# Optimization experiments

Measured on AMD Instinct MI355X. Metric: run time of the kernel, lower is better.

The kernel has to match this reference:

```python
import jax, jax.numpy as jnp
import numpy as np

H = 768


def lstm_cell(x, h, c, Wih, Whh, b):
    # PyTorch LSTMCell gate order: i, f, g, o
    gates = x @ Wih.T + h @ Whh.T + b
    i, f, g, o = jnp.split(gates, 4, axis=-1)
    c = jax.nn.sigmoid(f) * c + jax.nn.sigmoid(i) * jnp.tanh(g)
    h = jax.nn.sigmoid(o) * jnp.tanh(c)
    return h, c


def run_lstm(x, Wih, Whh, b, reverse):
    B = x.shape[0]
    Hd = Whh.shape[1]
    def step(carry, xt):
        h, c = lstm_cell(xt, carry[0], carry[1], Wih, Whh, b)
        return (h, c), h
    init = (jnp.zeros((B, Hd), x.dtype), jnp.zeros((B, Hd), x.dtype))
    _, hs = jax.lax.scan(step, init, jnp.swapaxes(x, 0, 1), reverse=reverse)
    return jnp.swapaxes(hs, 0, 1)


def _forward(hidden_state, golds, lstm_Wih_f, lstm_Whh_f, lstm_b_f,
             lstm_Wih_b, lstm_Whh_b, lstm_b_b, subw_Wih, subw_Whh, subw_b,
             word_Wih, word_Whh, word_b, cls_W, cls_b):
    B, T, _ = hidden_state.shape
    dt = hidden_state.dtype
    out_f = run_lstm(hidden_state, lstm_Wih_f, lstm_Whh_f, lstm_b_f, False)
    out_b = run_lstm(hidden_state, lstm_Wih_b, lstm_Whh_b, lstm_b_b, True)
    lstm_out = jnp.concatenate([out_f, out_b], -1)  # [B, T, 2H]

    subw_map = jnp.array([1, 2, 2], dtype=jnp.int32)
    word_map = jnp.array([0, 1, 1], dtype=jnp.int32)
    bidx = jnp.arange(B)
    S1, S2 = 2 * T + 2, T + 1
    carry0 = (jnp.zeros((S1, B, H), dt), jnp.zeros((S1, B, H), dt), jnp.zeros((B,), jnp.int32),
              jnp.zeros((S2, B, H), dt), jnp.zeros((S2, B, H), dt), jnp.zeros((B,), jnp.int32))
    xs = (jnp.swapaxes(lstm_out[:, :T - 1], 0, 1),  # features for subword cell at step idx-1
          jnp.swapaxes(lstm_out[:, 1:T], 0, 1),     # features concatenated into cls at step idx
          golds[:, 1:T].T.astype(jnp.int32))

    def step(carry, x):
        sh, sc, spos, wh, wc, wpos = carry
        x_prev, x_cur, g = x
        # subword stack-LSTM: read top-of-stack state, push new state at pos+1
        h1, c1 = lstm_cell(x_prev, sh[spos, bidx], sc[spos, bidx], subw_Wih, subw_Whh, subw_b)
        sh = sh.at[spos + 1, bidx].set(h1)
        sc = sc.at[spos + 1, bidx].set(c1)
        subword = jnp.concatenate([h1, c1], -1)  # [B, 2H] input to word stack-LSTM
        # word stack-LSTM
        h2, c2 = lstm_cell(subword, wh[wpos, bidx], wc[wpos, bidx], word_Wih, word_Whh, word_b)
        wh = wh.at[wpos + 1, bidx].set(h2)
        wc = wc.at[wpos + 1, bidx].set(c2)
        out = jnp.concatenate([h2, x_cur], -1) @ cls_W.T + cls_b  # [B, 2]
        # training path: ops from gold actions
        sop = subw_map[g]
        wop = word_map[g]
        spos = jnp.where(sop == 1, spos + 1, 0)      # APP: push; SEP: clear subword stack
        wpos = jnp.where(wop == 1, wpos + 1, wpos)   # SEP: push word; APP: hold
        return (sh, sc, spos, wh, wc, wpos), out

    _, outs = jax.lax.scan(step, carry0, xs)  # [T-1, B, 2]
    pred0 = jnp.broadcast_to(jnp.asarray([-1.0, 1.0], dt), (1, B, 2))
    return jnp.swapaxes(jnp.concatenate([pred0, outs], 0), 0, 1)  # [B, T, 2]


def setup_inputs() -> dict:
    key = jax.random.key(0)
    ks = jax.random.split(key, 12)
    B, T = 64, 256
    s = 0.02
    W = lambda k, shape: jax.random.normal(k, shape, jnp.float32) * s
    return {
        "hidden_state": jax.random.normal(ks[0], (B, T, H), jnp.float32),
        "golds": jax.random.randint(ks[1], (B, T), 0, 2),
        "lstm_Wih_f": W(ks[2], (4 * H, H)), "lstm_Whh_f": W(ks[3], (4 * H, H)), "lstm_b_f": jnp.zeros((4 * H,), jnp.float32),
        "lstm_Wih_b": W(ks[4], (4 * H, H)), "lstm_Whh_b": W(ks[5], (4 * H, H)), "lstm_b_b": jnp.zeros((4 * H,), jnp.float32),
        "subw_Wih": W(ks[6], (4 * H, 2 * H)), "subw_Whh": W(ks[7], (4 * H, H)), "subw_b": jnp.zeros((4 * H,), jnp.float32),
        "word_Wih": W(ks[8], (4 * H, 2 * H)), "word_Whh": W(ks[9], (4 * H, H)), "word_b": jnp.zeros((4 * H,), jnp.float32),
        "cls_W": W(ks[10], (2, 3 * H)), "cls_b": jnp.zeros((2,), jnp.float32),
    }


def reference(hidden_state, golds, lstm_Wih_f, lstm_Whh_f, lstm_b_f,
              lstm_Wih_b, lstm_Whh_b, lstm_b_b, subw_Wih, subw_Whh, subw_b,
              word_Wih, word_Whh, word_b, cls_W, cls_b):
    return _forward(hidden_state, golds, lstm_Wih_f, lstm_Whh_f, lstm_b_f,
                    lstm_Wih_b, lstm_Whh_b, lstm_b_b, subw_Wih, subw_Whh, subw_b,
                    word_Wih, word_Whh, word_b, cls_W, cls_b)
```

## Files before the change

### kernel.cpp

```cpp
#include <hip/hip_runtime.h>
#include <hip/hip_bf16.h>

typedef __attribute__((ext_vector_type(8))) short bf16x8;
typedef __attribute__((ext_vector_type(4))) float f32x4;
typedef __attribute__((ext_vector_type(4))) unsigned u32x4;

#define HD   768
#define NB   64
#define NT   256
#define NGATE 3072
#define FPAD 32

__device__ __forceinline__ float fast_sig(float x) { return 1.f / (1.f + __expf(-x)); }
__device__ __forceinline__ float fast_tanh(float x) {
  float t = __expf(-2.f * fabsf(x));
  float r = (1.f - t) / (1.f + t);
  return x < 0.f ? -r : r;
}
__device__ __forceinline__ float bf2f(unsigned short u) {
  union { unsigned i; float f; } v; v.i = ((unsigned)u) << 16; return v.f;
}
__device__ __forceinline__ unsigned short f2bfu(float f) {
  union { __hip_bfloat16 b; unsigned short u; } c;
  c.b = __float2bfloat16(f);
  return c.u;
}
__device__ __forceinline__ unsigned pack2(float a, float b) {
  return (unsigned)f2bfu(a) | ((unsigned)f2bfu(b) << 16);
}

#define VMW(N) do { asm volatile("s_waitcnt vmcnt(" #N ")" ::: "memory"); \
                    __builtin_amdgcn_sched_barrier(0); } while (0)

__device__ __forceinline__ int aload(int* p) {
  return __hip_atomic_load(p, __ATOMIC_RELAXED, __HIP_MEMORY_SCOPE_AGENT);
}
__device__ __forceinline__ void ustore(unsigned* p, unsigned v) {
  __hip_atomic_store(p, v, __ATOMIC_RELAXED, __HIP_MEMORY_SCOPE_AGENT);
}
__device__ __forceinline__ u32x4 cload16(const char* p) {
  u32x4 r;
  asm volatile("global_load_dwordx4 %0, %1, off sc0 sc1"
               : "=v"(r) : "v"(p) : "memory");
  return r;
}

__device__ __forceinline__ void arrive_flag(int* f) {
  asm volatile("s_waitcnt vmcnt(0)" ::: "memory");
  __syncthreads();
  if (threadIdx.x == 0)
    __hip_atomic_fetch_add(f, 1, __ATOMIC_RELAXED, __HIP_MEMORY_SCOPE_AGENT);
}

__device__ __forceinline__ void wait2(int* fa, int ta, int* fb, int tb) {
  int tid = threadIdx.x;
  int* p = nullptr; int tgt = 0;
  if (tid < 96)                            { p = fa + tid * FPAD;         tgt = ta; }
  else if (fb && tid >= 128 && tid < 224)  { p = fb + (tid - 128) * FPAD; tgt = tb; }
  if (p && tgt > 0) {
    int guard = 0;
    while (aload(p) < tgt) {
      __builtin_amdgcn_s_sleep(1);
      if (++guard > (1 << 17)) break;
    }
  }
  __syncthreads();
}

__device__ __forceinline__ int frag_dw(int b, int j) {
  return (((((j >> 5) * 4 + (b >> 4)) * 4 + ((j >> 3) & 3)) * 16 + (b & 15)) * 4)
         + ((j & 7) >> 1);
}

__device__ __forceinline__ int wswz(int r) {
  return ((r & 7) << 4) | (((r >> 3) & 3) << 7);
}

__device__ __forceinline__ void load_W_lds(unsigned short* Wl,
                                           const __hip_bfloat16* Wg,
                                           int n_base, int K)
{
  int chunksPerRow = (K * 2) / 16;
  int total = 32 * chunksPerRow;
  for (int idx = threadIdx.x; idx < total; idx += 256) {
    int r  = idx / chunksPerRow;
    int cb = (idx % chunksPerRow) * 16;
    bf16x8 v = *(const bf16x8*)((const char*)(Wg + (long)(n_base + r) * K) + cb);
    *(bf16x8*)((char*)Wl + (long)r * (K * 2) + (cb ^ wswz(r))) = v;
  }
}

__device__ __forceinline__ void mfma_cached(
    const __hip_bfloat16* a0p, int kbase, int NIT,
    const char* w0, const char* w1, int xr0, int xr1, int kk,
    f32x4& acc0, f32x4& acc1)
{
  #pragma unroll 4
  for (int it = kbase; it < kbase + NIT; ++it) {
    bf16x8 av = *(const bf16x8*)(a0p + it * 32 + kk);
    int oo = (it * 32 + kk) * 2;
    bf16x8 bv0 = *(const bf16x8*)(w0 + (oo ^ xr0));
    bf16x8 bv1 = *(const bf16x8*)(w1 + (oo ^ xr1));
    acc0 = __builtin_amdgcn_mfma_f32_16x16x32_bf16(av, bv0, acc0, 0, 0, 0);
    acc1 = __builtin_amdgcn_mfma_f32_16x16x32_bf16(av, bv1, acc1, 0, 0, 0);
  }
}

__device__ __forceinline__ void issue12(u32x4* dst, const char* base, int c0) {
  #pragma unroll
  for (int i = 0; i < 12; ++i)
    dst[i] = cload16(base + (size_t)(c0 + i) * 4096);
}

__device__ __forceinline__ void mfma_st12(
    const u32x4* st, int kbase,
    const char* w0, const char* w1, int xr0, int xr1, int kk,
    f32x4& acc0, f32x4& acc1)
{
  #pragma unroll
  for (int i = 0; i < 12; ++i) {
    int oo = ((kbase + i) * 32 + kk) * 2;
    bf16x8 av = __builtin_bit_cast(bf16x8, st[i]);
    bf16x8 bv0 = *(const bf16x8*)(w0 + (oo ^ xr0));
    bf16x8 bv1 = *(const bf16x8*)(w1 + (oo ^ xr1));
    acc0 = __builtin_amdgcn_mfma_f32_16x16x32_bf16(av, bv0, acc0, 0, 0, 0);
    acc1 = __builtin_amdgcn_mfma_f32_16x16x32_bf16(av, bv1, acc1, 0, 0, 0);
  }
}

__device__ __forceinline__ void pack_seg(const float* Wih, const float* Whh,
                                         __hip_bfloat16* dst, int Kih,
                                         long id0, long stride)
{
  int K = Kih + HD;
  long total = (long)NGATE * K;
  for (long idx = id0; idx < total; idx += stride) {
    int np = (int)(idx / K), k = (int)(idx % K);
    int j = np >> 2, g = np & 3;
    int n = g * HD + j;
    float v = (k < Kih) ? Wih[(long)n * Kih + k] : Whh[(long)n * HD + (k - Kih)];
    dst[idx] = __float2bfloat16(v);
  }
}

__global__ void setup_kernel(
    const float* __restrict__ x,
    const float* __restrict__ WihF, const float* __restrict__ WhhF,
    const float* __restrict__ WihB, const float* __restrict__ WhhB,
    const float* __restrict__ WihS, const float* __restrict__ WhhS,
    const float* __restrict__ WihW, const float* __restrict__ WhhW,
    __hip_bfloat16* __restrict__ X16,
    __hip_bfloat16* __restrict__ WF, __hip_bfloat16* __restrict__ WB,
    __hip_bfloat16* __restrict__ WS, __hip_bfloat16* __restrict__ WW)
{
  long id0 = (long)blockIdx.x * blockDim.x + threadIdx.x;
  long stride = (long)gridDim.x * blockDim.x;
  for (long i = id0; i < (long)NB * NT * HD; i += stride)
    X16[i] = __float2bfloat16(x[i]);
  pack_seg(WihF, WhhF, WF, 768, id0, stride);
  pack_seg(WihB, WhhB, WB, 768, id0, stride);
  pack_seg(WihS, WhhS, WS, 1536, id0, stride);
  pack_seg(WihW, WhhW, WW, 1536, id0, stride);
}

__global__ void fill_sentinel(float* out, int n, float v)
{
  int i = blockIdx.x * blockDim.x + threadIdx.x;
  if (i < n) out[i] = v;
}

__global__ __launch_bounds__(256, 1) void bilstm_persist(
    const __hip_bfloat16* __restrict__ X16,
    const __hip_bfloat16* __restrict__ WF,
    const __hip_bfloat16* __restrict__ WB,
    const float* __restrict__ bF, const float* __restrict__ bB,
    unsigned* __restrict__ H16u,
    __hip_bfloat16* __restrict__ L16,
    int* __restrict__ flags)
{
  __shared__ unsigned short Wl[32 * 1536];
  __shared__ float gl[64][33];
  int blk = blockIdx.x, dir = blk / 96, nt = blk % 96;
  load_W_lds(Wl, dir ? WB : WF, nt * 32, 1536);
  const float* bias = dir ? bB : bF;
  int* myflags = flags + dir * 96 * FPAD;
  int tid = threadIdx.x;
  unsigned* L16u = (unsigned*)L16;

  int w = tid >> 6, l = tid & 63, lr = l & 15, lh = l >> 4;
  const char* w0 = (const char*)Wl + lr * 3072;
  const char* w1 = (const char*)Wl + (16 + lr) * 3072;
  int xr0 = wswz(lr), xr1 = wswz(16 + lr);
  int kk = 8 * lh;
  int bA = 16 * w + lr;

  int e0 = tid * 2;
  int b = e0 >> 3, jj = e0 & 7;
  int j0 = nt * 8 + jj;
  float bv[2][4];
  #pragma unroll
  for (int u = 0; u < 2; ++u) {
    bv[u][0] = bias[j0 + u];          bv[u][1] = bias[HD + j0 + u];
    bv[u][2] = bias[2 * HD + j0 + u]; bv[u][3] = bias[3 * HD + j0 + u];
  }
  int fdw = frag_dw(b, j0);
  float cst[2] = {0.f, 0.f};
  __syncthreads();

  for (int s = 0; s < NT; ++s) {
    int par = s & 1;
    int t = dir ? (NT - 1 - s) : s;
    const __hip_bfloat16* xb = X16 + (long)t * HD + (long)bA * (NT * HD);
    f32x4 acc0 = {0.f, 0.f, 0.f, 0.f};
    f32x4 acc1 = {0.f, 0.f, 0.f, 0.f};
    mfma_cached(xb, 0, 12, w0, w1, xr0, xr1, kk, acc0, acc1);
    if (s > 0) wait2(myflags, s, nullptr, 0);
    const char* fpH = (const char*)(H16u + (long)(par * 2 + dir) * 24576)
                      + (size_t)(w * 64 + l) * 16;
    u32x4 hA[12], hB[12];
    issue12(hA, fpH, 0);
    issue12(hB, fpH, 12);
    mfma_cached(xb, 12, 12, w0, w1, xr0, xr1, kk, acc0, acc1);
    VMW(0);
    mfma_st12(hA, 24, w0, w1, xr0, xr1, kk, acc0, acc1);
    mfma_st12(hB, 36, w0, w1, xr0, xr1, kk, acc0, acc1);
    #pragma unroll
    for (int r = 0; r < 4; ++r) {
      gl[16 * w + 4 * lh + r][lr]      = acc0[r];
      gl[16 * w + 4 * lh + r][16 + lr] = acc1[r];
    }
    __syncthreads();
    float hv[2];
    #pragma unroll
    for (int u = 0; u < 2; ++u) {
      int col = 4 * (jj + u);
      float vi = gl[b][col + 0] + bv[u][0];
      float vf = gl[b][col + 1] + bv[u][1];
      float vg = gl[b][col + 2] + bv[u][2];
      float vo = gl[b][col + 3] + bv[u][3];
      float si = fast_sig(vi), sf = fast_sig(vf), so = fast_sig(vo);
      float tg = fast_tanh(vg);
      float c = sf * cst[u] + si * tg;
      cst[u] = c;
      hv[u] = so * fast_tanh(c);
    }
    unsigned pk = pack2(hv[0], hv[1]);
    ustore(H16u + (long)((par ^ 1) * 2 + dir) * 24576 + fdw, pk);
    L16u[((long)b * NT + t) * 768 + dir * 384 + (j0 >> 1)] = pk;
    if (s < NT - 1) arrive_flag(myflags + nt * FPAD);
  }
}

__global__ __launch_bounds__(256) void clsx_kernel(
    const __hip_bfloat16* __restrict__ L16,
    const float* __restrict__ clsW, const float* __restrict__ clsb,
    float* __restrict__ out)
{
  int t = blockIdx.x;
  int tid = threadIdx.x;
  int b = tid >> 2, o = (tid >> 1) & 1, hh = tid & 1;
  if (t == 0) {
    if (hh == 0) out[((long)b * NT) * 2 + o] = o ? 1.f : -1.f;
    return;
  }
  const bf16x8* xp = (const bf16x8*)(L16 + ((long)b * NT + t) * 1536 + hh * 768);
  const float* wv = clsW + o * 2304 + HD + hh * 768;
  float s = 0.f;
  for (int k = 0; k < 96; ++k) {
    bf16x8 v = xp[k];
    #pragma unroll
    for (int e = 0; e < 8; ++e)
      s += bf2f((unsigned short)v[e]) * wv[k * 8 + e];
  }
  s += __shfl_down(s, 1);
  if (hh == 0) out[((long)b * NT + t) * 2 + o] = s + clsb[o];
}

__global__ __launch_bounds__(256, 1) void stack_persist(
    const __hip_bfloat16* __restrict__ L16,
    const __hip_bfloat16* __restrict__ WS,
    const __hip_bfloat16* __restrict__ WW,
    const float* __restrict__ bS, const float* __restrict__ bW,
    const int* __restrict__ golds,
    const float* __restrict__ clsW,
    unsigned* __restrict__ H1Su,
    unsigned* __restrict__ H2Su,
    unsigned* __restrict__ SUBWu,
    float* __restrict__ out,
    int* __restrict__ flags)
{
  __shared__ unsigned short Wl[32 * 2304];
  __shared__ float gl[64][33];
  int blk = blockIdx.x, role = blk / 96, nt = blk % 96;
  int* flagS = flags + 2 * 96 * FPAD;
  int* flagW = flags + 3 * 96 * FPAD;
  const float* bias = role ? bW : bS;
  load_W_lds(Wl, role ? WW : WS, nt * 32, 2304);
  int tid = threadIdx.x;

  int w = tid >> 6, l = tid & 63, lr = l & 15, lh = l >> 4;
  const char* w0 = (const char*)Wl + lr * 4608;
  const char* w1 = (const char*)Wl + (16 + lr) * 4608;
  int xr0 = wswz(lr), xr1 = wswz(16 + lr);
  int kk = 8 * lh;
  int bA = 16 * w + lr;

  int e0 = tid * 2;
  int b = e0 >> 3, jj = e0 & 7;
  int j0 = nt * 8 + jj;
  float bv[2][4];
  #pragma unroll
  for (int u = 0; u < 2; ++u) {
    bv[u][0] = bias[j0 + u];          bv[u][1] = bias[HD + j0 + u];
    bv[u][2] = bias[2 * HD + j0 + u]; bv[u][3] = bias[3 * HD + j0 + u];
  }
  const int* gp = golds + b * NT + 1;
  int fdw_h = frag_dw(b, j0);
  float cst[2] = {0.f, 0.f};
  float hreg[2] = {0.f, 0.f};
  __syncthreads();

  if (role == 0) {
    int fdw_c = frag_dw(b, 768 + j0);
    for (int s = 0; s < NT - 1; ++s) {
      int g = gp[s];
      const __hip_bfloat16* lb = L16 + (long)s * 1536 + (long)bA * (NT * 1536);
      f32x4 acc0 = {0.f, 0.f, 0.f, 0.f};
      f32x4 acc1 = {0.f, 0.f, 0.f, 0.f};
      mfma_cached(lb, 0, 24, w0, w1, xr0, xr1, kk, acc0, acc1);
      wait2(flagS, s, flagW, s - 3);
      const char* fpH1 = (const char*)(H1Su + (long)(s & 1) * 24576)
                         + (size_t)(w * 64 + l) * 16;
      u32x4 hA[12], hB[12];
      issue12(hA, fpH1, 0);
      issue12(hB, fpH1, 12);
      mfma_cached(lb, 24, 24, w0, w1, xr0, xr1, kk, acc0, acc1);
      VMW(0);
      mfma_st12(hA, 48, w0, w1, xr0, xr1, kk, acc0, acc1);
      mfma_st12(hB, 60, w0, w1, xr0, xr1, kk, acc0, acc1);
      #pragma unroll
      for (int r = 0; r < 4; ++r) {
        gl[16 * w + 4 * lh + r][lr]      = acc0[r];
        gl[16 * w + 4 * lh + r][16 + lr] = acc1[r];
      }
      __syncthreads();
      float h1v[2], c1v[2];
      #pragma unroll
      for (int u = 0; u < 2; ++u) {
        int col = 4 * (jj + u);
        float vi = gl[b][col + 0] + bv[u][0];
        float vf = gl[b][col + 1] + bv[u][1];
        float vg = gl[b][col + 2] + bv[u][2];
        float vo = gl[b][col + 3] + bv[u][3];
        float si = fast_sig(vi), sf = fast_sig(vf), so = fast_sig(vo);
        float tg = fast_tanh(vg);
        c1v[u] = sf * cst[u] + si * tg;
        h1v[u] = so * fast_tanh(c1v[u]);
      }
      bool push = (g == 0);
      unsigned pkh = pack2(h1v[0], h1v[1]);
      unsigned pkc = pack2(c1v[0], c1v[1]);
      unsigned* sb = SUBWu + (long)(s & 3) * 49152;
      ustore(sb + fdw_h, pkh);
      ustore(sb + fdw_c, pkc);
      ustore(H1Su + (long)((s + 1) & 1) * 24576 + fdw_h, push ? pkh : 0u);
      cst[0] = push ? c1v[0] : 0.f;
      cst[1] = push ? c1v[1] : 0.f;
      arrive_flag(flagS + nt * FPAD);
    }
  } else {
    float cw0[2], cw1[2];
    #pragma unroll
    for (int u = 0; u < 2; ++u) { cw0[u] = clsW[j0 + u]; cw1[u] = clsW[2304 + j0 + u]; }
    for (int s = 0; s < NT - 1; ++s) {
      int g = gp[s];
      wait2(flagW, s, nullptr, 0);
      const char* fpH = (const char*)(H2Su + (long)(s & 1) * 24576)
                        + (size_t)(w * 64 + l) * 16;
      const char* fpS = (const char*)(SUBWu + (long)(s & 3) * 49152)
                        + (size_t)(w * 64 + l) * 16;
      u32x4 sA[12], sB[12], sC[12];
      issue12(sA, fpH, 0);
      issue12(sB, fpH, 12);
      wait2(flagS, s + 1, nullptr, 0);
      issue12(sC, fpS, 0);
      f32x4 acc0 = {0.f, 0.f, 0.f, 0.f};
      f32x4 acc1 = {0.f, 0.f, 0.f, 0.f};
      VMW(24);
      mfma_st12(sA, 48, w0, w1, xr0, xr1, kk, acc0, acc1);
      issue12(sA, fpS, 12);
      VMW(24);
      mfma_st12(sB, 60, w0, w1, xr0, xr1, kk, acc0, acc1);
      issue12(sB, fpS, 24);
      VMW(24);
      mfma_st12(sC, 0, w0, w1, xr0, xr1, kk, acc0, acc1);
      issue12(sC, fpS, 36);
      VMW(24);
      mfma_st12(sA, 12, w0, w1, xr0, xr1, kk, acc0, acc1);
      VMW(12);
      mfma_st12(sB, 24, w0, w1, xr0, xr1, kk, acc0, acc1);
      VMW(0);
      mfma_st12(sC, 36, w0, w1, xr0, xr1, kk, acc0, acc1);
      #pragma unroll
      for (int r = 0; r < 4; ++r) {
        gl[16 * w + 4 * lh + r][lr]      = acc0[r];
        gl[16 * w + 4 * lh + r][16 + lr] = acc1[r];
      }
      __syncthreads();
      float p0 = 0.f, p1 = 0.f;
      float h2v[2], c2v[2];
      #pragma unroll
      for (int u = 0; u < 2; ++u) {
        int col = 4 * (jj + u);
        float vi = gl[b][col + 0] + bv[u][0];
        float vf = gl[b][col + 1] + bv[u][1];
        float vg = gl[b][col + 2] + bv[u][2];
        float vo = gl[b][col + 3] + bv[u][3];
        float si = fast_sig(vi), sf = fast_sig(vf), so = fast_sig(vo);
        float tg = fast_tanh(vg);
        c2v[u] = sf * cst[u] + si * tg;
        h2v[u] = so * fast_tanh(c2v[u]);
        p0 += h2v[u] * cw0[u];
        p1 += h2v[u] * cw1[u];
      }
      bool push = (g >= 1);
      #pragma unroll
      for (int u = 0; u < 2; ++u) {
        cst[u]  = push ? c2v[u] : cst[u];
        hreg[u] = push ? h2v[u] : hreg[u];
      }
      ustore(H2Su + (long)((s + 1) & 1) * 24576 + fdw_h, pack2(hreg[0], hreg[1]));
      p0 += __shfl_down(p0, 1); p1 += __shfl_down(p1, 1);
      p0 += __shfl_down(p0, 2); p1 += __shfl_down(p1, 2);
      if ((tid & 3) == 0) {
        int bb = tid >> 2;
        atomicAdd(&out[((long)bb * NT + s + 1) * 2 + 0], p0);
        atomicAdd(&out[((long)bb * NT + s + 1) * 2 + 1], p1);
      }
      if (s < NT - 2) arrive_flag(flagW + nt * FPAD);
    }
  }
}

extern "C" void kernel_launch(void* const* d_in, const int* in_sizes, int n_in,
                              void* d_out, int out_size, void* d_ws, size_t ws_size,
                              hipStream_t stream)
{
  const float* x     = (const float*)d_in[0];
  const int*   golds = (const int*)d_in[1];
  const float* WihF  = (const float*)d_in[2];
  const float* WhhF  = (const float*)d_in[3];
  const float* bF    = (const float*)d_in[4];
  const float* WihB  = (const float*)d_in[5];
  const float* WhhB  = (const float*)d_in[6];
  const float* bB    = (const float*)d_in[7];
  const float* WihS  = (const float*)d_in[8];
  const float* WhhS  = (const float*)d_in[9];
  const float* bS    = (const float*)d_in[10];
  const float* WihW  = (const float*)d_in[11];
  const float* WhhW  = (const float*)d_in[12];
  const float* bW    = (const float*)d_in[13];
  const float* clsW  = (const float*)d_in[14];
  const float* clsb  = (const float*)d_in[15];
  float* out = (float*)d_out;

  const size_t OFF_X16  = 0;
  const size_t OFF_WF   = 25165824;
  const size_t OFF_WB   = 34603008;
  const size_t OFF_WS   = 44040192;
  const size_t OFF_WW   = 58195968;
  const size_t OFF_L16  = 72351744;
  const size_t OFF_H16  = 122683392;
  const size_t OFF_H1S  = 123076608;
  const size_t OFF_H2S  = 123273216;
  const size_t OFF_SUBW = 123469824;
  const size_t OFF_FLG  = 124256256;
  const size_t WS_NEEDED = 124305408;

  if (ws_size < WS_NEEDED) {
    fill_sentinel<<<(out_size + 255) / 256, 256, 0, stream>>>(out, out_size, 12345.f);
    return;
  }

  char* ws = (char*)d_ws;
  __hip_bfloat16* X16  = (__hip_bfloat16*)(ws + OFF_X16);
  __hip_bfloat16* WF   = (__hip_bfloat16*)(ws + OFF_WF);
  __hip_bfloat16* WB   = (__hip_bfloat16*)(ws + OFF_WB);
  __hip_bfloat16* WSp  = (__hip_bfloat16*)(ws + OFF_WS);
  __hip_bfloat16* WWp  = (__hip_bfloat16*)(ws + OFF_WW);
  __hip_bfloat16* L16  = (__hip_bfloat16*)(ws + OFF_L16);
  unsigned*       H16u = (unsigned*)(ws + OFF_H16);
  unsigned*       H1Su = (unsigned*)(ws + OFF_H1S);
  unsigned*       H2Su = (unsigned*)(ws + OFF_H2S);
  unsigned*       SUBWu= (unsigned*)(ws + OFF_SUBW);
  int*            flags= (int*)(ws + OFF_FLG);

  setup_kernel<<<4096, 256, 0, stream>>>(x, WihF, WhhF, WihB, WhhB,
                                         WihS, WhhS, WihW, WhhW,
                                         X16, WF, WB, WSp, WWp);
  hipMemsetAsync(ws + OFF_H16, 0, WS_NEEDED - OFF_H16, stream);

  bilstm_persist<<<192, 256, 0, stream>>>(X16, WF, WB, bF, bB, H16u, L16, flags);

  clsx_kernel<<<NT, 256, 0, stream>>>(L16, clsW, clsb, out);

  stack_persist<<<192, 256, 0, stream>>>(L16, WSp, WWp, bS, bW, golds, clsW,
                                         H1Su, H2Su, SUBWu, out, flags);
}
```

Before: 4.145 ms.

## Fuse classifier into stack kernel with extra reducer blocks, replace atomics with partial buffer

Removes the separate clsx_kernel launch and folds its work into 64 extra blocks of stack_persist. Those blocks compute the lstm_out classifier term and then reduce per-step partial logits from a new OUTC buffer, replacing the atomicAdd accumulation. The buffer reuses the X16 workspace region. The recurrent h-fragment loads are also restructured into a double-buffered mfma_frag helper. The aim is to cut a launch and atomic contention, but the reducer blocks poll flags and add occupancy pressure alongside the persistent blocks.

Result: faster. 3.884 ms (-6.3%).

```diff
diff --git a/kernel.cpp b/kernel.cpp
--- a/kernel.cpp
+++ b/kernel.cpp
@@ -38,9 +38,18 @@
 __device__ __forceinline__ void ustore(unsigned* p, unsigned v) {
   __hip_atomic_store(p, v, __ATOMIC_RELAXED, __HIP_MEMORY_SCOPE_AGENT);
 }
+__device__ __forceinline__ void ustore64(unsigned long long* p, unsigned long long v) {
+  __hip_atomic_store(p, v, __ATOMIC_RELAXED, __HIP_MEMORY_SCOPE_AGENT);
+}
 __device__ __forceinline__ u32x4 cload16(const char* p) {
   u32x4 r;
   asm volatile("global_load_dwordx4 %0, %1, off sc0 sc1"
+               : "=v"(r) : "v"(p) : "memory");
+  return r;
+}
+__device__ __forceinline__ unsigned cload4(const char* p) {
+  unsigned r;
+  asm volatile("global_load_dword %0, %1, off sc0 sc1"
                : "=v"(r) : "v"(p) : "memory");
   return r;
 }
@@ -67,6 +76,18 @@
   __syncthreads();
 }
 
+__device__ __forceinline__ void wait_coarse(int* fa, int t) {
+  int tid = threadIdx.x;
+  if (tid < 96) {
+    int guard = 0;
+    while (aload(fa + tid * FPAD) < t) {
+      __builtin_amdgcn_s_sleep(127);
+      if (++guard > (1 << 15)) break;
+    }
+  }
+  __syncthreads();
+}
+
 __device__ __forceinline__ int frag_dw(int b, int j) {
   return (((((j >> 5) * 4 + (b >> 4)) * 4 + ((j >> 3) & 3)) * 16 + (b & 15)) * 4)
          + ((j & 7) >> 1);
@@ -103,6 +124,40 @@
     bf16x8 bv1 = *(const bf16x8*)(w1 + (oo ^ xr1));
     acc0 = __builtin_amdgcn_mfma_f32_16x16x32_bf16(av, bv0, acc0, 0, 0, 0);
     acc1 = __builtin_amdgcn_mfma_f32_16x16x32_bf16(av, bv1, acc1, 0, 0, 0);
+  }
+}
+
+template<int CF>
+__device__ __forceinline__ void mfma_frag(
+    const char* Fbase, int l, int w,
+    const char* w0, const char* w1, int xr0, int xr1, int kk, int kbase,
+    f32x4& acc0, f32x4& acc1)
+{
+  const char* fp = Fbase + (size_t)(w * 64 + l) * 16;
+  u32x4 st[2][12];
+  #pragma unroll
+  for (int i = 0; i < 12; ++i)
+    st[0][i] = cload16(fp + (size_t)i * 4096);
+  #pragma unroll
+  for (int c = 0; c < CF / 12; ++c) {
+    if (c + 1 < CF / 12) {
+      #pragma unroll
+      for (int i = 0; i < 12; ++i)
+        st[(c + 1) & 1][i] = cload16(fp + (size_t)((c + 1) * 12 + i) * 4096);
+      asm volatile("s_waitcnt vmcnt(12)" ::: "memory");
+    } else {
+      asm volatile("s_waitcnt vmcnt(0)" ::: "memory");
+    }
+    __builtin_amdgcn_sched_barrier(0);
+    #pragma unroll
+    for (int i = 0; i < 12; ++i) {
+      int oo = ((kbase + c * 12 + i) * 32 + kk) * 2;
+      bf16x8 av = __builtin_bit_cast(bf16x8, st[c & 1][i]);
+      bf16x8 bv0 = *(const bf16x8*)(w0 + (oo ^ xr0));
+      bf16x8 bv1 = *(const bf16x8*)(w1 + (oo ^ xr1));
+      acc0 = __builtin_amdgcn_mfma_f32_16x16x32_bf16(av, bv0, acc0, 0, 0, 0);
+      acc1 = __builtin_amdgcn_mfma_f32_16x16x32_bf16(av, bv1, acc1, 0, 0, 0);
+    }
   }
 }
 
@@ -210,20 +265,13 @@
   for (int s = 0; s < NT; ++s) {
     int par = s & 1;
     int t = dir ? (NT - 1 - s) : s;
-    const __hip_bfloat16* xb = X16 + (long)t * HD + (long)bA * (NT * HD);
     f32x4 acc0 = {0.f, 0.f, 0.f, 0.f};
     f32x4 acc1 = {0.f, 0.f, 0.f, 0.f};
-    mfma_cached(xb, 0, 12, w0, w1, xr0, xr1, kk, acc0, acc1);
+    mfma_cached(X16 + (long)t * HD + (long)bA * (NT * HD), 0, 24,
+                w0, w1, xr0, xr1, kk, acc0, acc1);
     if (s > 0) wait2(myflags, s, nullptr, 0);
-    const char* fpH = (const char*)(H16u + (long)(par * 2 + dir) * 24576)
-                      + (size_t)(w * 64 + l) * 16;
-    u32x4 hA[12], hB[12];
-    issue12(hA, fpH, 0);
-    issue12(hB, fpH, 12);
-    mfma_cached(xb, 12, 12, w0, w1, xr0, xr1, kk, acc0, acc1);
-    VMW(0);
-    mfma_st12(hA, 24, w0, w1, xr0, xr1, kk, acc0, acc1);
-    mfma_st12(hB, 36, w0, w1, xr0, xr1, kk, acc0, acc1);
+    mfma_frag<24>((const char*)(H16u + (long)(par * 2 + dir) * 24576),
+                  l, w, w0, w1, xr0, xr1, kk, 24, acc0, acc1);
     #pragma unroll
     for (int r = 0; r < 4; ++r) {
       gl[16 * w + 4 * lh + r][lr]      = acc0[r];
@@ -251,41 +299,17 @@
   }
 }
 
-__global__ __launch_bounds__(256) void clsx_kernel(
-    const __hip_bfloat16* __restrict__ L16,
-    const float* __restrict__ clsW, const float* __restrict__ clsb,
-    float* __restrict__ out)
-{
-  int t = blockIdx.x;
-  int tid = threadIdx.x;
-  int b = tid >> 2, o = (tid >> 1) & 1, hh = tid & 1;
-  if (t == 0) {
-    if (hh == 0) out[((long)b * NT) * 2 + o] = o ? 1.f : -1.f;
-    return;
-  }
-  const bf16x8* xp = (const bf16x8*)(L16 + ((long)b * NT + t) * 1536 + hh * 768);
-  const float* wv = clsW + o * 2304 + HD + hh * 768;
-  float s = 0.f;
-  for (int k = 0; k < 96; ++k) {
-    bf16x8 v = xp[k];
-    #pragma unroll
-    for (int e = 0; e < 8; ++e)
-      s += bf2f((unsigned short)v[e]) * wv[k * 8 + e];
-  }
-  s += __shfl_down(s, 1);
-  if (hh == 0) out[((long)b * NT + t) * 2 + o] = s + clsb[o];
-}
-
 __global__ __launch_bounds__(256, 1) void stack_persist(
     const __hip_bfloat16* __restrict__ L16,
     const __hip_bfloat16* __restrict__ WS,
     const __hip_bfloat16* __restrict__ WW,
     const float* __restrict__ bS, const float* __restrict__ bW,
     const int* __restrict__ golds,
-    const float* __restrict__ clsW,
+    const float* __restrict__ clsW, const float* __restrict__ clsb,
     unsigned* __restrict__ H1Su,
     unsigned* __restrict__ H2Su,
     unsigned* __restrict__ SUBWu,
+    float* __restrict__ OUTC,
     float* __restrict__ out,
     int* __restrict__ flags)
 {
@@ -294,9 +318,73 @@
   int blk = blockIdx.x, role = blk / 96, nt = blk % 96;
   int* flagS = flags + 2 * 96 * FPAD;
   int* flagW = flags + 3 * 96 * FPAD;
+  int tid = threadIdx.x;
+
+  if (role == 2) {
+    int q = blk - 192;
+    int b = tid >> 2, o = (tid >> 1) & 1, hh = tid & 1;
+    #pragma unroll
+    for (int i = 0; i < 4; ++i) {
+      int t = q * 4 + i;
+      if (t == 0) {
+        if (hh == 0) out[((long)b * NT) * 2 + o] = o ? 1.f : -1.f;
+      } else {
+        const bf16x8* xp = (const bf16x8*)(L16 + ((long)b * NT + t) * 1536 + hh * 768);
+        const float* wv = clsW + o * 2304 + HD + hh * 768;
+        float s = 0.f;
+        for (int k = 0; k < 96; ++k) {
+          bf16x8 v = xp[k];
+          #pragma unroll
+          for (int e = 0; e < 8; ++e)
+            s += bf2f((unsigned short)v[e]) * wv[k * 8 + e];
+        }
+        s += __shfl_down(s, 1);
+        if (hh == 0) out[((long)b * NT + t) * 2 + o] = s + clsb[o];
+      }
+    }
+    for (int i = 0; i < 4; ++i) {
+      int t = q * 4 + i;
+      if (t < 1) continue;
+      int sstep = t - 1;
+      wait_coarse(flagW, t);
+      if (tid < 128) {
+        const char* bp = (const char*)OUTC + (((size_t)sstep * 96) * 128 + tid) * 4;
+        float acc = 0.f;
+        unsigned bufA[12], bufB[12];
+        #pragma unroll
+        for (int k = 0; k < 12; ++k) bufA[k] = cload4(bp + (size_t)k * 512);
+        #pragma unroll
+        for (int c = 0; c < 8; ++c) {
+          if (c + 1 < 8) {
+            if ((c & 1) == 0) {
+              #pragma unroll
+              for (int k = 0; k < 12; ++k)
+                bufB[k] = cload4(bp + (size_t)((c + 1) * 12 + k) * 512);
+            } else {
+              #pragma unroll
+              for (int k = 0; k < 12; ++k)
+                bufA[k] = cload4(bp + (size_t)((c + 1) * 12 + k) * 512);
+            }
+            VMW(12);
+          } else {
+            VMW(0);
+          }
+          if ((c & 1) == 0) {
+            #pragma unroll
+            for (int k = 0; k < 12; ++k) acc += __builtin_bit_cast(float, bufA[k]);
+          } else {
+            #pragma unroll
+            for (int k = 0; k < 12; ++k) acc += __builtin_bit_cast(float, bufB[k]);
+          }
+        }
+        out[((long)(tid >> 1) * NT + t) * 2 + (tid & 1)] += acc;
+      }
+    }
+    return;
+  }
+
   const float* bias = role ? bW : bS;
   load_W_lds(Wl, role ? WW : WS, nt * 32, 2304);
-  int tid = threadIdx.x;
 
   int w = tid >> 6, l = tid & 63, lr = l & 15, lh = l >> 4;
   const char* w0 = (const char*)Wl + lr * 4608;
@@ -329,15 +417,9 @@
       f32x4 acc1 = {0.f, 0.f, 0.f, 0.f};
       mfma_cached(lb, 0, 24, w0, w1, xr0, xr1, kk, acc0, acc1);
       wait2(flagS, s, flagW, s - 3);
-      const char* fpH1 = (const char*)(H1Su + (long)(s & 1) * 24576)
-                         + (size_t)(w * 64 + l) * 16;
-      u32x4 hA[12], hB[12];
-      issue12(hA, fpH1, 0);
-      issue12(hB, fpH1, 12);
       mfma_cached(lb, 24, 24, w0, w1, xr0, xr1, kk, acc0, acc1);
-      VMW(0);
-      mfma_st12(hA, 48, w0, w1, xr0, xr1, kk, acc0, acc1);
-      mfma_st12(hB, 60, w0, w1, xr0, xr1, kk, acc0, acc1);
+      mfma_frag<24>((const char*)(H1Su + (long)(s & 1) * 24576),
+                    l, w, w0, w1, xr0, xr1, kk, 48, acc0, acc1);
       #pragma unroll
       for (int r = 0; r < 4; ++r) {
         gl[16 * w + 4 * lh + r][lr]      = acc0[r];
@@ -434,10 +516,12 @@
       p0 += __shfl_down(p0, 2); p1 += __shfl_down(p1, 2);
       if ((tid & 3) == 0) {
         int bb = tid >> 2;
-        atomicAdd(&out[((long)bb * NT + s + 1) * 2 + 0], p0);
-        atomicAdd(&out[((long)bb * NT + s + 1) * 2 + 1], p1);
-      }
-      if (s < NT - 2) arrive_flag(flagW + nt * FPAD);
+        union { float f[2]; unsigned long long u; } pkc;
+        pkc.f[0] = p0; pkc.f[1] = p1;
+        ustore64((unsigned long long*)&OUTC[(((size_t)s * 96) + nt) * 128 + bb * 2],
+                 pkc.u);
+      }
+      arrive_flag(flagW + nt * FPAD);
     }
   }
 }
@@ -493,6 +577,7 @@
   unsigned*       H1Su = (unsigned*)(ws + OFF_H1S);
   unsigned*       H2Su = (unsigned*)(ws + OFF_H2S);
   unsigned*       SUBWu= (unsigned*)(ws + OFF_SUBW);
+  float*          OUTC = (float*)(ws + OFF_X16);
   int*            flags= (int*)(ws + OFF_FLG);
 
   setup_kernel<<<4096, 256, 0, stream>>>(x, WihF, WhhF, WihB, WhhB,
@@ -502,8 +587,7 @@
 
   bilstm_persist<<<192, 256, 0, stream>>>(X16, WF, WB, bF, bB, H16u, L16, flags);
 
-  clsx_kernel<<<NT, 256, 0, stream>>>(L16, clsW, clsb, out);
-
-  stack_persist<<<192, 256, 0, stream>>>(L16, WSp, WWp, bS, bW, golds, clsW,
-                                         H1Su, H2Su, SUBWu, out, flags);
-}
+  stack_persist<<<256, 256, 0, stream>>>(L16, WSp, WWp, bS, bW, golds,
+                                         clsW, clsb, H1Su, H2Su, SUBWu,
+                                         OUTC, out, flags);
+}
```
